# Performance work log

Hardware: AMD Instinct MI355X
Metric: run time of the kernel (lower is better)

## Reference

```python
import jax, jax.numpy as jnp
import numpy as np


def setup_inputs() -> dict:
    key = jax.random.key(0)
    images = jax.random.uniform(key, (64, 384, 384, 3), dtype=jnp.float32)
    return {"images": images, "k": 5}


def reference(images, k):
    # cv2.dilate with a k x k kernel of ones == per-channel max filter with SAME padding.
    # Applied over the whole batch in one fused reduce_window (window only over H, W).
    out = jax.lax.reduce_window(
        images,
        -jnp.inf,
        jax.lax.max,
        window_dimensions=(1, k, k, 1),
        window_strides=(1, 1, 1, 1),
        padding="SAME",
    )
    # cv_to_tf appends a trailing singleton dim before tf.stack -> (B, H, W, C, 1)
    return out[..., None]
```

## Files before the change

kernel.cpp:

```cpp
#include <hip/hip_runtime.h>
#include <hip/hip_bf16.h>


#define Bn 64
#define H 384
#define ROWF 1152
#define ROWBYTES (ROWF * 4)
#define WF4 288
#define RB 12
#define NLOAD (RB + 4)
#define GROUPS 8
#define STRIPS 5
#define SOUT 60
#define NEGINF (-3.402823466e+38f)

__device__ __forceinline__ float4 max4(float4 a, float4 b) {
  return make_float4(fmaxf(a.x, b.x), fmaxf(a.y, b.y),
                     fmaxf(a.z, b.z), fmaxf(a.w, b.w));
}
__device__ __forceinline__ float4 shflup4(float4 v, int d) {
  return make_float4(__shfl_up(v.x, d), __shfl_up(v.y, d),
                     __shfl_up(v.z, d), __shfl_up(v.w, d));
}
__device__ __forceinline__ float4 shfldn4(float4 v, int d) {
  return make_float4(__shfl_down(v.x, d), __shfl_down(v.y, d),
                     __shfl_down(v.z, d), __shfl_down(v.w, d));
}

__global__ __launch_bounds__(256) void dilate5_kernel(
    const float* __restrict__ in, float* __restrict__ out) {
  const int wv = threadIdx.x >> 6;
  const int lane = threadIdx.x & 63;
  int t = blockIdx.x;
  const int strip = t % STRIPS; t /= STRIPS;
  const int grp = t % GROUPS;   t /= GROUPS;
  const int b = t;

  const int row0 = (grp * 4 + wv) * RB;
  const int col = strip * SOUT - 2 + lane;
  const bool cvalid = (col >= 0) && (col < WF4);
  const int ccl = col < 0 ? 0 : (col > WF4 - 1 ? WF4 - 1 : col);
  const size_t coff = (size_t)ccl * 16;
  const bool willstore = (lane >= 2) && (lane < 62) && (col < WF4);

  const float4 ninf = make_float4(NEGINF, NEGINF, NEGINF, NEGINF);
  const char* __restrict__ imgb = (const char*)in + (size_t)b * H * ROWBYTES;
  char* __restrict__ outb = (char*)out + (size_t)b * H * ROWBYTES;

  float4 raw[NLOAD];
#pragma unroll
  for (int j = 0; j < NLOAD; ++j) {
    int gh = row0 - 2 + j;
    int ghc = gh < 0 ? 0 : (gh > H - 1 ? H - 1 : gh);
    raw[j] = *reinterpret_cast<const float4*>(imgb + (size_t)ghc * ROWBYTES + coff);
  }

  auto hcomb = [&](int gh, float4 Cv) -> float4 {
    if (!cvalid) Cv = ninf;
    float4 A = shflup4(Cv, 2);
    float4 Bv = shflup4(Cv, 1);
    float4 D = shfldn4(Cv, 1);
    float4 E = shfldn4(Cv, 2);
    float4 h;
    h.x = fmaxf(fmaxf(fmaxf(A.z, Bv.y), fmaxf(Cv.x, Cv.w)), D.z);
    h.y = fmaxf(fmaxf(fmaxf(A.w, Bv.z), fmaxf(Cv.y, D.x)), D.w);
    h.z = fmaxf(fmaxf(fmaxf(Bv.x, Bv.w), fmaxf(Cv.z, D.y)), E.x);
    h.w = fmaxf(fmaxf(fmaxf(Bv.y, Cv.x), fmaxf(Cv.w, D.z)), E.y);
    if (gh < 0 || gh >= H) h = ninf;
    return h;
  };

  float4 r0 = hcomb(row0 - 2, raw[0]);
  float4 r1 = hcomb(row0 - 1, raw[1]);
  float4 r2 = hcomb(row0,     raw[2]);
  float4 r3 = hcomb(row0 + 1, raw[3]);

#pragma unroll
  for (int i = 0; i < RB; ++i) {
    const int o = row0 + i;
    float4 r4 = hcomb(o + 2, raw[i + 4]);
    float4 v = max4(max4(max4(r0, r1), max4(r2, r3)), r4);
    if (willstore)
      *reinterpret_cast<float4*>(outb + (size_t)o * ROWBYTES + coff) = v;
    r0 = r1; r1 = r2; r2 = r3; r3 = r4;
  }
}

extern "C" void kernel_launch(void* const* d_in, const int* in_sizes, int n_in,
                              void* d_out, int out_size, void* d_ws, size_t ws_size,
                              hipStream_t stream) {
  const float* images = (const float*)d_in[0];
  float* out = (float*)d_out;
  const int nblocks = Bn * GROUPS * STRIPS;
  dilate5_kernel<<<nblocks, 256, 0, stream>>>(images, out);
}
```

Baseline: 198.5 us.

## Process all column strips per wave with fewer rows and software-pipelined row loads

Each wave now covers all five column strips of a row band of eight rows, instead of one strip over twelve rows, and the grid shrinks to batch times twelve blocks. Rows are loaded one ahead through a rolling register pipeline instead of preloading the whole band. A launch_bounds minimum of three blocks per CU is added. This cuts the vertical halo re-read fraction per strip and overlaps loads with compute, but raises register pressure and reduces block count, which may hurt latency hiding.

```diff
diff --git a/kernel.cpp b/kernel.cpp
--- a/kernel.cpp
+++ b/kernel.cpp
@@ -4,14 +4,12 @@
 
 #define Bn 64
 #define H 384
-#define ROWF 1152
-#define ROWBYTES (ROWF * 4)
+#define ROWBYTES 4608
 #define WF4 288
-#define RB 12
-#define NLOAD (RB + 4)
-#define GROUPS 8
-#define STRIPS 5
+#define RB 8
+#define NCH 5
 #define SOUT 60
+#define GRPS 12
 #define NEGINF (-3.402823466e+38f)
 
 __device__ __forceinline__ float4 max4(float4 a, float4 b) {
@@ -27,62 +25,86 @@
                      __shfl_down(v.z, d), __shfl_down(v.w, d));
 }
 
-__global__ __launch_bounds__(256) void dilate5_kernel(
+__global__ __launch_bounds__(256, 3) void dilate5_kernel(
     const float* __restrict__ in, float* __restrict__ out) {
   const int wv = threadIdx.x >> 6;
   const int lane = threadIdx.x & 63;
   int t = blockIdx.x;
-  const int strip = t % STRIPS; t /= STRIPS;
-  const int grp = t % GROUPS;   t /= GROUPS;
+  const int grp = t % GRPS; t /= GRPS;
   const int b = t;
+  const int row0 = (grp * 4 + wv) * RB;
 
-  const int row0 = (grp * 4 + wv) * RB;
-  const int col = strip * SOUT - 2 + lane;
-  const bool cvalid = (col >= 0) && (col < WF4);
-  const int ccl = col < 0 ? 0 : (col > WF4 - 1 ? WF4 - 1 : col);
-  const size_t coff = (size_t)ccl * 16;
-  const bool willstore = (lane >= 2) && (lane < 62) && (col < WF4);
-
-  const float4 ninf = make_float4(NEGINF, NEGINF, NEGINF, NEGINF);
   const char* __restrict__ imgb = (const char*)in + (size_t)b * H * ROWBYTES;
   char* __restrict__ outb = (char*)out + (size_t)b * H * ROWBYTES;
 
-  float4 raw[NLOAD];
+  int coff[NCH];
+  bool cval[NCH], smask[NCH];
 #pragma unroll
-  for (int j = 0; j < NLOAD; ++j) {
-    int gh = row0 - 2 + j;
-    int ghc = gh < 0 ? 0 : (gh > H - 1 ? H - 1 : gh);
-    raw[j] = *reinterpret_cast<const float4*>(imgb + (size_t)ghc * ROWBYTES + coff);
+  for (int k = 0; k < NCH; ++k) {
+    const int col = SOUT * k - 2 + lane;
+    cval[k] = (col >= 0) && (col < WF4);
+    const int ccl = col < 0 ? 0 : (col >= WF4 ? WF4 - 1 : col);
+    coff[k] = ccl * 16;
+    smask[k] = (lane >= 2) && (lane < 62) && (col < WF4);
   }
+  const float4 ninf = make_float4(NEGINF, NEGINF, NEGINF, NEGINF);
 
-  auto hcomb = [&](int gh, float4 Cv) -> float4 {
-    if (!cvalid) Cv = ninf;
-    float4 A = shflup4(Cv, 2);
-    float4 Bv = shflup4(Cv, 1);
-    float4 D = shfldn4(Cv, 1);
-    float4 E = shfldn4(Cv, 2);
-    float4 h;
-    h.x = fmaxf(fmaxf(fmaxf(A.z, Bv.y), fmaxf(Cv.x, Cv.w)), D.z);
-    h.y = fmaxf(fmaxf(fmaxf(A.w, Bv.z), fmaxf(Cv.y, D.x)), D.w);
-    h.z = fmaxf(fmaxf(fmaxf(Bv.x, Bv.w), fmaxf(Cv.z, D.y)), E.x);
-    h.w = fmaxf(fmaxf(fmaxf(Bv.y, Cv.x), fmaxf(Cv.w, D.z)), E.y);
-    if (gh < 0 || gh >= H) h = ninf;
-    return h;
+  auto loadrow = [&](int gh, float4* dst) {
+    const int ghc = gh < 0 ? 0 : (gh > H - 1 ? H - 1 : gh);
+    const char* rb = imgb + (size_t)ghc * ROWBYTES;
+#pragma unroll
+    for (int k = 0; k < NCH; ++k)
+      dst[k] = *reinterpret_cast<const float4*>(rb + coff[k]);
   };
 
-  float4 r0 = hcomb(row0 - 2, raw[0]);
-  float4 r1 = hcomb(row0 - 1, raw[1]);
-  float4 r2 = hcomb(row0,     raw[2]);
-  float4 r3 = hcomb(row0 + 1, raw[3]);
+  auto hcombrow = [&](int gh, const float4* raw, float4* h) {
+    const bool rowok = (gh >= 0) && (gh < H);
+#pragma unroll
+    for (int k = 0; k < NCH; ++k) {
+      float4 Cv = cval[k] ? raw[k] : ninf;
+      float4 A = shflup4(Cv, 2);
+      float4 Bv = shflup4(Cv, 1);
+      float4 D = shfldn4(Cv, 1);
+      float4 E = shfldn4(Cv, 2);
+      float4 r;
+      r.x = fmaxf(fmaxf(fmaxf(A.z, Bv.y), fmaxf(Cv.x, Cv.w)), D.z);
+      r.y = fmaxf(fmaxf(fmaxf(A.w, Bv.z), fmaxf(Cv.y, D.x)), D.w);
+      r.z = fmaxf(fmaxf(fmaxf(Bv.x, Bv.w), fmaxf(Cv.z, D.y)), E.x);
+      r.w = fmaxf(fmaxf(fmaxf(Bv.y, Cv.x), fmaxf(Cv.w, D.z)), E.y);
+      h[k] = rowok ? r : ninf;
+    }
+  };
+
+  float4 t0[NCH], t1[NCH], t2[NCH], t3[NCH], cur[NCH], nxt[NCH];
+  loadrow(row0 - 2, t0);
+  loadrow(row0 - 1, t1);
+  loadrow(row0,     t2);
+  loadrow(row0 + 1, t3);
+  loadrow(row0 + 2, cur);
+
+  float4 r0[NCH], r1[NCH], r2[NCH], r3[NCH], r4[NCH];
+  hcombrow(row0 - 2, t0, r0);
+  hcombrow(row0 - 1, t1, r1);
+  hcombrow(row0,     t2, r2);
+  hcombrow(row0 + 1, t3, r3);
 
 #pragma unroll
   for (int i = 0; i < RB; ++i) {
     const int o = row0 + i;
-    float4 r4 = hcomb(o + 2, raw[i + 4]);
-    float4 v = max4(max4(max4(r0, r1), max4(r2, r3)), r4);
-    if (willstore)
-      *reinterpret_cast<float4*>(outb + (size_t)o * ROWBYTES + coff) = v;
-    r0 = r1; r1 = r2; r2 = r3; r3 = r4;
+    if (i + 1 < RB) loadrow(o + 3, nxt);
+    hcombrow(o + 2, cur, r4);
+    char* orow = outb + (size_t)o * ROWBYTES;
+#pragma unroll
+    for (int k = 0; k < NCH; ++k) {
+      float4 v = max4(max4(max4(r0[k], r1[k]), max4(r2[k], r3[k])), r4[k]);
+      if (smask[k])
+        *reinterpret_cast<float4*>(orow + coff[k]) = v;
+    }
+#pragma unroll
+    for (int k = 0; k < NCH; ++k) {
+      r0[k] = r1[k]; r1[k] = r2[k]; r2[k] = r3[k]; r3[k] = r4[k];
+      cur[k] = nxt[k];
+    }
   }
 }
 
@@ -91,6 +113,6 @@
                               hipStream_t stream) {
   const float* images = (const float*)d_in[0];
   float* out = (float*)d_out;
-  const int nblocks = Bn * GROUPS * STRIPS;
+  const int nblocks = Bn * GRPS;
   dilate5_kernel<<<nblocks, 256, 0, stream>>>(images, out);
 }
```

Measured after the change: 249.0 us. 1.25x slower.
